# Performance work log

Measured on AMD Instinct MI355X. Metric: run time of the kernel, lower is better.

## Reference

```python
import jax, jax.numpy as jnp
import numpy as np

AGENT_THRESH = 0.5
X_DIS_THRESH = 1.5
Y_DIS_THRESH = 3.0
DIS_THRESH = 3.0
LOSS_WEIGHT = 1.0
BIG = 1000000.0

B, A, M, T, C = 128, 2048, 6, 12, 10


def setup_inputs() -> dict:
    key = jax.random.key(0)
    k1, k2, k3, k4, k5 = jax.random.split(key, 5)
    return {
        "ego_fut_preds": jax.random.normal(k1, (B, T, 2), dtype=jnp.float32),
        "agent_preds": jax.random.normal(k2, (B, A, 2), dtype=jnp.float32),
        "agent_fut_preds": jax.random.normal(k3, (B, A, M, T, 2), dtype=jnp.float32),
        "agent_score_preds": jax.random.uniform(k4, (B, A, C), dtype=jnp.float32),
        "agent_fut_cls_preds": jax.random.normal(k5, (B, A, M), dtype=jnp.float32),
    }


def _plan_collision_loss(ego_fut_preds, agent_preds, agent_fut_preds,
                         agent_score_preds, agent_fut_cls_preds):
    # --- invalidate low-score / non-vehicle agents -------------------------
    max_score = jnp.max(agent_score_preds, axis=-1)           # [B, A]
    max_idx = jnp.argmax(agent_score_preds, axis=-1)          # [B, A]
    invalid = (max_score < AGENT_THRESH) | (max_idx > 4)      # [B, A]
    afp = jnp.where(invalid[:, :, None, None, None], BIG, agent_fut_preds)

    # --- select best mode per agent ---------------------------------------
    best_mode = jnp.argmax(agent_fut_cls_preds, axis=-1)      # [B, A]
    afp = jnp.take_along_axis(
        afp, best_mode[:, :, None, None, None], axis=2
    ).squeeze(2)                                              # [B, A, T, 2]

    # --- cumsum deltas -> trajectories -------------------------------------
    pred = jnp.cumsum(ego_fut_preds, axis=-2)                 # [B, T, 2]
    afp = jnp.cumsum(afp, axis=-2)                            # [B, A, T, 2]
    target = agent_preds[:, :, None, :] + afp                 # [B, A, T, 2]

    # --- pairwise distances, far-agent masking -----------------------------
    diff = pred[:, None, :, :] - target                       # [B, A, T, 2]
    dist = jnp.linalg.norm(diff, axis=-1)                     # [B, A, T]
    target = jnp.where((dist > DIS_THRESH)[..., None], BIG, target)

    x_dist = jnp.abs(pred[:, None, :, 0] - target[..., 0])    # [B, A, T]
    y_dist = jnp.abs(pred[:, None, :, 1] - target[..., 1])    # [B, A, T]

    # argmin over agents then gather == min over agents
    x_min = jnp.min(x_dist, axis=1)                           # [B, T]
    y_min = jnp.min(y_dist, axis=1)                           # [B, T]

    x_loss = jnp.where(x_min > X_DIS_THRESH, 0.0, X_DIS_THRESH - x_min)
    y_loss = jnp.where(y_min > Y_DIS_THRESH, 0.0, Y_DIS_THRESH - y_min)
    loss = jnp.stack([x_loss, y_loss], axis=-1)               # [B, T, 2]

    # reduction='mean', weight=None, avg_factor=None
    return LOSS_WEIGHT * jnp.mean(loss)


def reference(ego_fut_preds, agent_preds, agent_fut_preds,
              agent_score_preds, agent_fut_cls_preds):
    return _plan_collision_loss(ego_fut_preds, agent_preds, agent_fut_preds,
                                agent_score_preds, agent_fut_cls_preds)
```

## Files before the change

kernel.cpp:

```cpp
#include <hip/hip_runtime.h>

#define AGENT_THRESH 0.5f
#define X_DIS_THRESH 1.5f
#define Y_DIS_THRESH 3.0f
#define DIS2_THRESH  9.0f
#define LOSS_WEIGHT  1.0f
#define FLT_BIG      3.402823466e+38f

constexpr int B = 128, A = 2048, M = 6, T = 12, C = 10;
constexpr int APB = 256;
constexpr int CHUNKS = A / APB;
constexpr int NBLK = B * CHUNKS;
constexpr int SLOTS = T * 2;
constexpr int GRP = 10;

constexpr size_t WS_PARTIAL_OFF = (size_t)NBLK * SLOTS;
constexpr size_t WS_COUNTER_OFF = WS_PARTIAL_OFF + 128;

__global__ __launch_bounds__(APB) void pcl_main_kernel(
    const float* __restrict__ ego,
    const float* __restrict__ agent_preds,
    const float* __restrict__ afp,
    const float* __restrict__ scores,
    const float* __restrict__ cls,
    float* __restrict__ blockmins,
    unsigned int* __restrict__ counter)
{
    const int b     = blockIdx.x / CHUNKS;
    const int chunk = blockIdx.x % CHUNKS;
    const int tid   = threadIdx.x;
    const int a     = chunk * APB + tid;

    if (blockIdx.x == 0 && tid == 0) *counter = 0;

    __shared__ float egoraw[SLOTS];
    __shared__ float predx[T], predy[T];
    __shared__ float sred[APB][25];
    __shared__ float spart[SLOTS * GRP];

    const size_t ba = (size_t)b * A + a;

    const float2* sp2 = (const float2*)(scores + ba * C);
    float2 s0 = sp2[0], s1 = sp2[1], s2 = sp2[2], s3 = sp2[3], s4 = sp2[4];
    const float2* cp2 = (const float2*)(cls + ba * M);
    float2 c0 = cp2[0], c1 = cp2[1], c2 = cp2[2];
    const float2 apxy = ((const float2*)agent_preds)[ba];

    if (tid < SLOTS) egoraw[tid] = ego[(size_t)b * SLOTS + tid];
    __syncthreads();
    if (tid < SLOTS) {
        const int coord = (tid >= T) ? 1 : 0;
        const int tt    = tid - T * coord;
        float s = 0.f;
        for (int i = 0; i <= tt; ++i) s += egoraw[2 * i + coord];
        if (coord) predy[tt] = s; else predx[tt] = s;
    }
    __syncthreads();

    float sv[C] = {s0.x, s0.y, s1.x, s1.y, s2.x, s2.y, s3.x, s3.y, s4.x, s4.y};
    float ms = sv[0];
    int   mi = 0;
    #pragma unroll
    for (int c = 1; c < C; ++c)
        if (sv[c] > ms) { ms = sv[c]; mi = c; }
    const bool valid = (ms >= AGENT_THRESH) && (mi <= 4);

    float p[SLOTS];
    #pragma unroll
    for (int k = 0; k < SLOTS; ++k) p[k] = FLT_BIG;

    if (valid) {
        float cv[M] = {c0.x, c0.y, c1.x, c1.y, c2.x, c2.y};
        float mc = cv[0];
        int   mm = 0;
        #pragma unroll
        for (int m = 1; m < M; ++m)
            if (cv[m] > mc) { mc = cv[m]; mm = m; }

        const float4* fp = (const float4*)(afp + (ba * M + mm) * (size_t)SLOTS);
        float4 f0 = fp[0], f1 = fp[1], f2 = fp[2], f3 = fp[3], f4 = fp[4], f5 = fp[5];
        float dxv[SLOTS];
        dxv[0]=f0.x; dxv[1]=f0.y; dxv[2]=f0.z; dxv[3]=f0.w;
        dxv[4]=f1.x; dxv[5]=f1.y; dxv[6]=f1.z; dxv[7]=f1.w;
        dxv[8]=f2.x; dxv[9]=f2.y; dxv[10]=f2.z; dxv[11]=f2.w;
        dxv[12]=f3.x; dxv[13]=f3.y; dxv[14]=f3.z; dxv[15]=f3.w;
        dxv[16]=f4.x; dxv[17]=f4.y; dxv[18]=f4.z; dxv[19]=f4.w;
        dxv[20]=f5.x; dxv[21]=f5.y; dxv[22]=f5.z; dxv[23]=f5.w;

        float csx = 0.f, csy = 0.f;
        #pragma unroll
        for (int t = 0; t < T; ++t) {
            csx += dxv[2 * t + 0];
            csy += dxv[2 * t + 1];
            const float dx = predx[t] - (apxy.x + csx);
            const float dy = predy[t] - (apxy.y + csy);
            const bool hit = (dx * dx + dy * dy <= DIS2_THRESH);
            p[2 * t + 0] = fminf(p[2 * t + 0], hit ? fabsf(dx) : FLT_BIG);
            p[2 * t + 1] = fminf(p[2 * t + 1], hit ? fabsf(dy) : FLT_BIG);
        }
    }

    #pragma unroll
    for (int k = 0; k < SLOTS; ++k) sred[tid][k] = p[k];
    __syncthreads();

    if (tid < SLOTS * GRP) {
        const int s = tid % SLOTS;
        const int g = tid / SLOTS;
        float pm = FLT_BIG;
        for (int r = g; r < APB; r += GRP) pm = fminf(pm, sred[r][s]);
        spart[tid] = pm;
    }
    __syncthreads();

    if (tid < SLOTS) {
        float m = spart[tid];
        #pragma unroll
        for (int g = 1; g < GRP; ++g) m = fminf(m, spart[g * SLOTS + tid]);
        blockmins[(size_t)blockIdx.x * SLOTS + tid] = m;
    }
}

__global__ __launch_bounds__(192) void pcl_finalize_kernel(
    const float* __restrict__ blockmins,
    float* __restrict__ partial,
    unsigned int* __restrict__ counter,
    float* __restrict__ out)
{
    const int b   = blockIdx.x;
    const int tid = threadIdx.x;

    __shared__ float sv[CHUNKS * SLOTS];
    __shared__ float ssum[SLOTS];
    __shared__ bool  is_last;

    sv[tid] = blockmins[(size_t)b * CHUNKS * SLOTS + tid];
    __syncthreads();

    if (tid < SLOTS) {
        float m = sv[tid];
        #pragma unroll
        for (int c = 1; c < CHUNKS; ++c) m = fminf(m, sv[c * SLOTS + tid]);
        const float thr = (tid & 1) ? Y_DIS_THRESH : X_DIS_THRESH;
        ssum[tid] = (m > thr) ? 0.f : (thr - m);
    }
    __syncthreads();

    if (tid == 0) {
        float s = 0.f;
        #pragma unroll
        for (int k = 0; k < SLOTS; ++k) s += ssum[k];
        partial[b] = s;
        __threadfence();
        unsigned int prev = atomicAdd(counter, 1u);
        is_last = (prev == (unsigned int)(B - 1));
    }
    __syncthreads();

    if (is_last) {
        __threadfence();
        if (tid < 64) {
            volatile const float* vp = partial;
            float s = vp[tid] + vp[tid + 64];
            #pragma unroll
            for (int off = 32; off > 0; off >>= 1)
                s += __shfl_down(s, off, 64);
            if (tid == 0)
                out[0] = LOSS_WEIGHT * s / (float)(B * SLOTS);
        }
    }
}

extern "C" void kernel_launch(void* const* d_in, const int* in_sizes, int n_in,
                              void* d_out, int out_size, void* d_ws, size_t ws_size,
                              hipStream_t stream) {
    const float* ego         = (const float*)d_in[0];
    const float* agent_preds = (const float*)d_in[1];
    const float* afp         = (const float*)d_in[2];
    const float* scores      = (const float*)d_in[3];
    const float* cls         = (const float*)d_in[4];
    float* out               = (float*)d_out;

    float* blockmins         = (float*)d_ws;
    float* partial           = (float*)d_ws + WS_PARTIAL_OFF;
    unsigned int* counter    = (unsigned int*)((float*)d_ws + WS_COUNTER_OFF);

    pcl_main_kernel<<<NBLK, APB, 0, stream>>>(
        ego, agent_preds, afp, scores, cls, blockmins, counter);
    pcl_finalize_kernel<<<B, 192, 0, stream>>>(blockmins, partial, counter, out);
}
```

Before: 20.68 us.

## Fuse finalize into main kernel via last-block reduction and coalesce input staging

Merges the two launches into one kernel: each block writes its per-slot minima with atomics, and the last block to arrive (tracked by a monotonically increasing counter taken modulo the block count) computes the per-batch minima, thresholds, and the mean. Scores, class logits and agent positions are now staged into shared memory with coalesced float4 loads instead of strided per-thread float2 loads. This removes a kernel launch and improves load coalescing, at the cost of a serial final reduction over 128x8x24 values in a single block using atomic reads.

```diff
diff --git a/kernel.cpp b/kernel.cpp
--- a/kernel.cpp
+++ b/kernel.cpp
@@ -14,40 +14,46 @@
 constexpr int SLOTS = T * 2;
 constexpr int GRP = 10;
 
-constexpr size_t WS_PARTIAL_OFF = (size_t)NBLK * SLOTS;
-constexpr size_t WS_COUNTER_OFF = WS_PARTIAL_OFF + 128;
+constexpr int SMEM_F = 6656;
 
-__global__ __launch_bounds__(APB) void pcl_main_kernel(
+__global__ __launch_bounds__(APB) void pcl_fused_kernel(
     const float* __restrict__ ego,
     const float* __restrict__ agent_preds,
     const float* __restrict__ afp,
     const float* __restrict__ scores,
     const float* __restrict__ cls,
-    float* __restrict__ blockmins,
-    unsigned int* __restrict__ counter)
+    unsigned int* __restrict__ blockmins_u,
+    unsigned int* __restrict__ counter,
+    float* __restrict__ out)
 {
-    const int b     = blockIdx.x / CHUNKS;
-    const int chunk = blockIdx.x % CHUNKS;
+    const int bid   = blockIdx.x;
+    const int b     = bid / CHUNKS;
+    const int chunk = bid % CHUNKS;
     const int tid   = threadIdx.x;
-    const int a     = chunk * APB + tid;
+    const size_t base = (size_t)b * A + chunk * APB;
 
-    if (blockIdx.x == 0 && tid == 0) *counter = 0;
+    __shared__ float smem[SMEM_F];
+    __shared__ float egoraw[SLOTS], predx[T], predy[T];
+    __shared__ int slast;
 
-    __shared__ float egoraw[SLOTS];
-    __shared__ float predx[T], predy[T];
-    __shared__ float sred[APB][25];
-    __shared__ float spart[SLOTS * GRP];
-
-    const size_t ba = (size_t)b * A + a;
-
-    const float2* sp2 = (const float2*)(scores + ba * C);
-    float2 s0 = sp2[0], s1 = sp2[1], s2 = sp2[2], s3 = sp2[3], s4 = sp2[4];
-    const float2* cp2 = (const float2*)(cls + ba * M);
-    float2 c0 = cp2[0], c1 = cp2[1], c2 = cp2[2];
-    const float2 apxy = ((const float2*)agent_preds)[ba];
-
+    {
+        const float4* g = (const float4*)(scores + base * C);
+        float4* l = (float4*)&smem[0];
+        for (int i = tid; i < (APB * C) / 4; i += APB) l[i] = g[i];
+    }
+    {
+        const float4* g = (const float4*)(cls + base * M);
+        float4* l = (float4*)&smem[2560];
+        for (int i = tid; i < (APB * M) / 4; i += APB) l[i] = g[i];
+    }
+    {
+        const float4* g = (const float4*)(agent_preds + base * 2);
+        float4* l = (float4*)&smem[4096];
+        for (int i = tid; i < (APB * 2) / 4; i += APB) l[i] = g[i];
+    }
     if (tid < SLOTS) egoraw[tid] = ego[(size_t)b * SLOTS + tid];
     __syncthreads();
+
     if (tid < SLOTS) {
         const int coord = (tid >= T) ? 1 : 0;
         const int tt    = tid - T * coord;
@@ -55,9 +61,16 @@
         for (int i = 0; i <= tt; ++i) s += egoraw[2 * i + coord];
         if (coord) predy[tt] = s; else predx[tt] = s;
     }
+
+    float sv[C], cv[M];
+    #pragma unroll
+    for (int c = 0; c < C; ++c) sv[c] = smem[tid * C + c];
+    #pragma unroll
+    for (int m = 0; m < M; ++m) cv[m] = smem[2560 + tid * M + m];
+    const float apx = smem[4096 + tid * 2 + 0];
+    const float apy = smem[4096 + tid * 2 + 1];
     __syncthreads();
 
-    float sv[C] = {s0.x, s0.y, s1.x, s1.y, s2.x, s2.y, s3.x, s3.y, s4.x, s4.y};
     float ms = sv[0];
     int   mi = 0;
     #pragma unroll
@@ -70,13 +83,13 @@
     for (int k = 0; k < SLOTS; ++k) p[k] = FLT_BIG;
 
     if (valid) {
-        float cv[M] = {c0.x, c0.y, c1.x, c1.y, c2.x, c2.y};
         float mc = cv[0];
         int   mm = 0;
         #pragma unroll
         for (int m = 1; m < M; ++m)
             if (cv[m] > mc) { mc = cv[m]; mm = m; }
 
+        const size_t ba = base + tid;
         const float4* fp = (const float4*)(afp + (ba * M + mm) * (size_t)SLOTS);
         float4 f0 = fp[0], f1 = fp[1], f2 = fp[2], f3 = fp[3], f4 = fp[4], f5 = fp[5];
         float dxv[SLOTS];
@@ -92,8 +105,8 @@
         for (int t = 0; t < T; ++t) {
             csx += dxv[2 * t + 0];
             csy += dxv[2 * t + 1];
-            const float dx = predx[t] - (apxy.x + csx);
-            const float dy = predy[t] - (apxy.y + csy);
+            const float dx = predx[t] - (apx + csx);
+            const float dy = predy[t] - (apy + csy);
             const bool hit = (dx * dx + dy * dy <= DIS2_THRESH);
             p[2 * t + 0] = fminf(p[2 * t + 0], hit ? fabsf(dx) : FLT_BIG);
             p[2 * t + 1] = fminf(p[2 * t + 1], hit ? fabsf(dy) : FLT_BIG);
@@ -101,72 +114,58 @@
     }
 
     #pragma unroll
-    for (int k = 0; k < SLOTS; ++k) sred[tid][k] = p[k];
+    for (int k = 0; k < SLOTS; ++k) smem[tid * 25 + k] = p[k];
     __syncthreads();
 
     if (tid < SLOTS * GRP) {
         const int s = tid % SLOTS;
         const int g = tid / SLOTS;
         float pm = FLT_BIG;
-        for (int r = g; r < APB; r += GRP) pm = fminf(pm, sred[r][s]);
-        spart[tid] = pm;
+        for (int r = g; r < APB; r += GRP) pm = fminf(pm, smem[r * 25 + s]);
+        smem[6400 + tid] = pm;
     }
     __syncthreads();
 
     if (tid < SLOTS) {
-        float m = spart[tid];
+        float m = smem[6400 + tid];
         #pragma unroll
-        for (int g = 1; g < GRP; ++g) m = fminf(m, spart[g * SLOTS + tid]);
-        blockmins[(size_t)blockIdx.x * SLOTS + tid] = m;
-    }
-}
-
-__global__ __launch_bounds__(192) void pcl_finalize_kernel(
-    const float* __restrict__ blockmins,
-    float* __restrict__ partial,
-    unsigned int* __restrict__ counter,
-    float* __restrict__ out)
-{
-    const int b   = blockIdx.x;
-    const int tid = threadIdx.x;
-
-    __shared__ float sv[CHUNKS * SLOTS];
-    __shared__ float ssum[SLOTS];
-    __shared__ bool  is_last;
-
-    sv[tid] = blockmins[(size_t)b * CHUNKS * SLOTS + tid];
-    __syncthreads();
-
-    if (tid < SLOTS) {
-        float m = sv[tid];
-        #pragma unroll
-        for (int c = 1; c < CHUNKS; ++c) m = fminf(m, sv[c * SLOTS + tid]);
-        const float thr = (tid & 1) ? Y_DIS_THRESH : X_DIS_THRESH;
-        ssum[tid] = (m > thr) ? 0.f : (thr - m);
+        for (int g = 1; g < GRP; ++g) m = fminf(m, smem[6400 + g * SLOTS + tid]);
+        atomicExch(&blockmins_u[(size_t)bid * SLOTS + tid], __float_as_uint(m));
     }
     __syncthreads();
 
     if (tid == 0) {
-        float s = 0.f;
-        #pragma unroll
-        for (int k = 0; k < SLOTS; ++k) s += ssum[k];
-        partial[b] = s;
         __threadfence();
         unsigned int prev = atomicAdd(counter, 1u);
-        is_last = (prev == (unsigned int)(B - 1));
+        slast = ((prev % (unsigned)NBLK) == (unsigned)(NBLK - 1)) ? 1 : 0;
     }
     __syncthreads();
 
-    if (is_last) {
+    if (slast) {
         __threadfence();
-        if (tid < 64) {
-            volatile const float* vp = partial;
-            float s = vp[tid] + vp[tid + 64];
+        float s = 0.f;
+        for (int pi = tid; pi < B * SLOTS; pi += APB) {
+            const int bb = pi / SLOTS;
+            const int sl = pi % SLOTS;
+            unsigned int mu =
+                atomicAdd(&blockmins_u[((size_t)bb * CHUNKS + 0) * SLOTS + sl], 0u);
             #pragma unroll
-            for (int off = 32; off > 0; off >>= 1)
-                s += __shfl_down(s, off, 64);
-            if (tid == 0)
-                out[0] = LOSS_WEIGHT * s / (float)(B * SLOTS);
+            for (int c2 = 1; c2 < CHUNKS; ++c2) {
+                unsigned int v =
+                    atomicAdd(&blockmins_u[((size_t)bb * CHUNKS + c2) * SLOTS + sl], 0u);
+                mu = (v < mu) ? v : mu;
+            }
+            const float mv  = __uint_as_float(mu);
+            const float thr = (sl & 1) ? Y_DIS_THRESH : X_DIS_THRESH;
+            s += (mv > thr) ? 0.f : (thr - mv);
+        }
+        #pragma unroll
+        for (int off = 32; off > 0; off >>= 1) s += __shfl_down(s, off, 64);
+        if ((tid & 63) == 0) smem[6640 + (tid >> 6)] = s;
+        __syncthreads();
+        if (tid == 0) {
+            float tot = smem[6640] + smem[6641] + smem[6642] + smem[6643];
+            out[0] = LOSS_WEIGHT * tot / (float)(B * SLOTS);
         }
     }
 }
@@ -181,11 +180,9 @@
     const float* cls         = (const float*)d_in[4];
     float* out               = (float*)d_out;
 
-    float* blockmins         = (float*)d_ws;
-    float* partial           = (float*)d_ws + WS_PARTIAL_OFF;
-    unsigned int* counter    = (unsigned int*)((float*)d_ws + WS_COUNTER_OFF);
+    unsigned int* blockmins_u = (unsigned int*)d_ws;
+    unsigned int* counter     = (unsigned int*)d_ws + NBLK * SLOTS + 32;
 
-    pcl_main_kernel<<<NBLK, APB, 0, stream>>>(
-        ego, agent_preds, afp, scores, cls, blockmins, counter);
-    pcl_finalize_kernel<<<B, 192, 0, stream>>>(blockmins, partial, counter, out);
+    pcl_fused_kernel<<<NBLK, APB, 0, stream>>>(
+        ego, agent_preds, afp, scores, cls, blockmins_u, counter, out);
 }
```

Result: slower. 36.97 us (+78.7%).
